# Performance work log

Measured on AMD Instinct MI355X. Metric: run time of the kernel, lower is better.

## Reference

```python
import jax, jax.numpy as jnp
import numpy as np

N_NODES = 1_000_000
N_EDGES = 33_554_432


def setup_inputs() -> dict:
    key = jax.random.key(0)
    k1, k2, k3, k4, k5 = jax.random.split(key, 5)
    node_features = jax.random.normal(k1, (N_NODES,), dtype=jnp.float32)
    edge_index = jax.random.randint(k2, (2, N_EDGES), 0, N_NODES, dtype=jnp.int64)
    cycle_mask = jax.random.uniform(k3, (N_EDGES,), dtype=jnp.float32)
    W = jax.random.normal(k4, (1, 3), dtype=jnp.float32) * 0.5
    b = jax.random.normal(k5, (1,), dtype=jnp.float32) * 0.1
    min_sum_scaler = jnp.array([0.8], dtype=jnp.float32)
    cycle_penalty = jnp.array([-1.0], dtype=jnp.float32)
    return {
        "node_features": node_features,
        "edge_index": edge_index,
        "cycle_mask": cycle_mask,
        "W": W,
        "b": b,
        "min_sum_scaler": min_sum_scaler,
        "cycle_penalty": cycle_penalty,
    }


def reference(node_features, edge_index, cycle_mask, W, b, min_sum_scaler, cycle_penalty):
    src, dst = edge_index[0], edge_index[1]
    x_src = node_features[src]                      # [E] gather
    x_dst = node_features[dst]                      # [E] gather
    # Linear(3,1) over [x_src, x_dst, cycle_mask]: expand the tiny GEMM as fused elementwise
    raw = x_src * W[0, 0] + x_dst * W[0, 1] + cycle_mask * W[0, 2] + b[0]
    raw = jax.nn.leaky_relu(raw, negative_slope=0.01)
    raw = raw + cycle_mask * cycle_penalty[0]
    attention_weights = jax.nn.sigmoid(raw)
    messages = x_src * attention_weights * min_sum_scaler[0]   # [E]
    out = jax.ops.segment_sum(messages, dst, num_segments=node_features.shape[0])
    return out
```

## Files before the change

kernel.cpp:

```cpp
#include <hip/hip_runtime.h>
#include <hip/hip_bf16.h>


#define THREADS 256
#define NBLK    1024
#define NBUCK   256
#define BSH     12
#define NPB     (1 << BSH)
#define TILE    4096
#define NPAD    (NBUCK << BSH)

typedef unsigned int uint4e __attribute__((ext_vector_type(4)));

__device__ __forceinline__ float edge_msg(float xs, float xd, float cc,
                                          float W0, float W1, float W2,
                                          float bb, float ms, float cp) {
    float raw = fmaf(xs, W0, fmaf(xd, W1, fmaf(cc, W2, bb)));
    raw = (raw > 0.0f) ? raw : 0.01f * raw;
    raw = fmaf(cc, cp, raw);
    const float att = __builtin_amdgcn_rcpf(1.0f + __expf(-raw));
    return xs * att * ms;
}

__global__ __launch_bounds__(THREADS) void p1_hist(
    const int* __restrict__ dsts, int E, int epb,
    unsigned int* __restrict__ histT)
{
    __shared__ unsigned int h[4][NBUCK];
    const int t = threadIdx.x;
#pragma unroll
    for (int w = 0; w < 4; ++w) h[w][t] = 0u;
    __syncthreads();

    const int wid   = t >> 6;
    const int blk   = blockIdx.x;
    const int start = blk * epb;
    const int end   = min(E, start + epb);
    const int n     = end - start;
    const int nvec  = n >> 2;

    for (int i = t; i < nvec; i += THREADS) {
        const int4 d4 = *(const int4*)(dsts + start + (i << 2));
        atomicAdd(&h[wid][d4.x >> BSH], 1u);
        atomicAdd(&h[wid][d4.y >> BSH], 1u);
        atomicAdd(&h[wid][d4.z >> BSH], 1u);
        atomicAdd(&h[wid][d4.w >> BSH], 1u);
    }
    for (int e = start + (nvec << 2) + t; e < end; e += THREADS)
        atomicAdd(&h[wid][dsts[e] >> BSH], 1u);

    __syncthreads();
    histT[(size_t)t * NBLK + blk] = h[0][t] + h[1][t] + h[2][t] + h[3][t];
}

__global__ __launch_bounds__(THREADS) void p_scan1(
    unsigned int* __restrict__ histT, unsigned int* __restrict__ totals)
{
    const int b = blockIdx.x;
    unsigned int* row = histT + (size_t)b * NBLK;
    const int t = threadIdx.x;

    uint4 c = *(uint4*)(row + (t << 2));
    const unsigned s1 = c.x;
    const unsigned s2 = c.x + c.y;
    const unsigned s3 = s2 + c.z;
    const unsigned tsum = s3 + c.w;

    __shared__ unsigned int ls[THREADS];
    ls[t] = tsum;
    __syncthreads();
    for (int off = 1; off < THREADS; off <<= 1) {
        unsigned tmp = 0u;
        if (t >= off) tmp = ls[t - off];
        __syncthreads();
        if (t >= off) ls[t] += tmp;
        __syncthreads();
    }
    const unsigned base = (t == 0) ? 0u : ls[t - 1];

    uint4 o;
    o.x = base; o.y = base + s1; o.z = base + s2; o.w = base + s3;
    *(uint4*)(row + (t << 2)) = o;
    if (t == 0) totals[b] = ls[THREADS - 1];
}

__global__ __launch_bounds__(NBUCK) void p_scan2(
    const unsigned int* __restrict__ totals, unsigned int* __restrict__ bucketBase)
{
    __shared__ unsigned int ls[NBUCK];
    const int t = threadIdx.x;
    ls[t] = totals[t];
    __syncthreads();
    for (int off = 1; off < NBUCK; off <<= 1) {
        unsigned tmp = 0u;
        if (t >= off) tmp = ls[t - off];
        __syncthreads();
        if (t >= off) ls[t] += tmp;
        __syncthreads();
    }
    bucketBase[t] = (t == 0) ? 0u : ls[t - 1];
}

__global__ __launch_bounds__(THREADS) void p2_partition(
    const int*   __restrict__ srcs,
    const int*   __restrict__ dsts,
    const float* __restrict__ cm,
    const unsigned int* __restrict__ relT,
    const unsigned int* __restrict__ bucketBase,
    uint2* __restrict__ recs, int E, int epb)
{
    __shared__ unsigned int cur[NBUCK];
    __shared__ unsigned int hist[NBUCK];
    __shared__ unsigned int scanT[NBUCK];
    __shared__ unsigned int rankCur[NBUCK];
    __shared__ unsigned int delta[NBUCK];
    __shared__ uint2        buf[TILE];
    __shared__ unsigned int slotArr[TILE];

    const int blk = blockIdx.x;
    const int t   = threadIdx.x;
    cur[t] = bucketBase[t] + relT[(size_t)t * NBLK + blk];

    const int start = blk * epb;
    const int end   = min(E, start + epb);

    for (int t0 = start; t0 < end; t0 += TILE) {
        const int n    = min(end - t0, TILE);
        const int nvec = n >> 2;

        hist[t] = 0u;
        __syncthreads();
        for (int i = t; i < nvec; i += THREADS) {
            const int4 d4 = *(const int4*)(dsts + t0 + (i << 2));
            atomicAdd(&hist[d4.x >> BSH], 1u);
            atomicAdd(&hist[d4.y >> BSH], 1u);
            atomicAdd(&hist[d4.z >> BSH], 1u);
            atomicAdd(&hist[d4.w >> BSH], 1u);
        }
        for (int e = t0 + (nvec << 2) + t; e < t0 + n; e += THREADS)
            atomicAdd(&hist[dsts[e] >> BSH], 1u);
        __syncthreads();

        scanT[t] = hist[t];
        __syncthreads();
        for (int off = 1; off < NBUCK; off <<= 1) {
            unsigned v = 0u;
            if (t >= off) v = scanT[t - off];
            __syncthreads();
            if (t >= off) scanT[t] += v;
            __syncthreads();
        }
        {
            const unsigned excl = scanT[t] - hist[t];
            rankCur[t] = excl;
            delta[t]   = cur[t] - excl;
        }
        __syncthreads();

        for (int i = t; i < nvec; i += THREADS) {
            const int base = t0 + (i << 2);
            const int4   s4 = *(const int4*)  (srcs + base);
            const int4   d4 = *(const int4*)  (dsts + base);
            const float4 c4 = *(const float4*)(cm   + base);
            const unsigned s[4] = {(unsigned)s4.x, (unsigned)s4.y, (unsigned)s4.z, (unsigned)s4.w};
            const unsigned d[4] = {(unsigned)d4.x, (unsigned)d4.y, (unsigned)d4.z, (unsigned)d4.w};
            const float    c[4] = {c4.x, c4.y, c4.z, c4.w};
#pragma unroll
            for (int k = 0; k < 4; ++k) {
                const unsigned b = d[k] >> BSH;
                const unsigned r = atomicAdd(&rankCur[b], 1u);
                buf[r] = make_uint2((s[k] << BSH) | (d[k] & (NPB - 1u)),
                                    __float_as_uint(c[k]));
                slotArr[r] = r + delta[b];
            }
        }
        for (int e = t0 + (nvec << 2) + t; e < t0 + n; e += THREADS) {
            const unsigned dv = (unsigned)dsts[e];
            const unsigned b  = dv >> BSH;
            const unsigned r  = atomicAdd(&rankCur[b], 1u);
            buf[r] = make_uint2(((unsigned)srcs[e] << BSH) | (dv & (NPB - 1u)),
                                __float_as_uint(cm[e]));
            slotArr[r] = r + delta[b];
        }
        __syncthreads();

        for (int j = t; j < n; j += THREADS)
            recs[slotArr[j]] = buf[j];
        __syncthreads();
        cur[t] += hist[t];
        __syncthreads();
    }
}

__global__ __launch_bounds__(THREADS) void p3_reduce(
    const uint2* __restrict__ recs,
    const unsigned int* __restrict__ totals,
    const unsigned int* __restrict__ bucketBase,
    const float* __restrict__ nf, int N, int nslice,
    const float* __restrict__ Wp, const float* __restrict__ bp,
    const float* __restrict__ msp, const float* __restrict__ cpp_,
    float* __restrict__ partials)
{
    __shared__ float acc[NPB];
    __shared__ float nfw[NPB];
    const int b = blockIdx.x / nslice;
    const int s = blockIdx.x % nslice;
    const int t = threadIdx.x;
    const int nbase = b << BSH;

    for (int j = t; j < NPB; j += THREADS) {
        acc[j] = 0.0f;
        const int g = nbase + j;
        nfw[j] = (g < N) ? nf[g] : 0.0f;
    }
    __syncthreads();

    const float W0 = Wp[0], W1 = Wp[1], W2 = Wp[2];
    const float bb = bp[0], ms = msp[0], cp = cpp_[0];

    const unsigned cnt   = totals[b];
    const unsigned base  = bucketBase[b];
    const unsigned chunk = (cnt + (unsigned)nslice - 1u) / (unsigned)nslice;
    unsigned k0 = min(cnt, (unsigned)s * chunk);
    unsigned k1 = min(cnt, k0 + chunk);
    unsigned g0 = base + k0, g1 = base + k1;

    if ((g0 & 1u) && g0 < g1) {
        if (t == 0) {
            const uint2 r = recs[g0];
            const unsigned dl = r.x & (NPB - 1u);
            atomicAdd(&acc[dl], edge_msg(nf[r.x >> BSH], nfw[dl],
                                         __uint_as_float(r.y),
                                         W0, W1, W2, bb, ms, cp));
        }
        ++g0;
    }
    if (g0 < g1 && ((g1 - g0) & 1u)) {
        --g1;
        if (t == 0) {
            const uint2 r = recs[g1];
            const unsigned dl = r.x & (NPB - 1u);
            atomicAdd(&acc[dl], edge_msg(nf[r.x >> BSH], nfw[dl],
                                         __uint_as_float(r.y),
                                         W0, W1, W2, bb, ms, cp));
        }
    }

    const unsigned npair = (g1 > g0) ? ((g1 - g0) >> 1) : 0u;
    const unsigned noct  = npair >> 2;

    for (unsigned p = t; p < noct; p += THREADS) {
        const uint2* rp = recs + g0 + (p << 3);
        const uint4e qa = __builtin_nontemporal_load((const uint4e*)(rp));
        const uint4e qb = __builtin_nontemporal_load((const uint4e*)(rp + 2));
        const uint4e qc = __builtin_nontemporal_load((const uint4e*)(rp + 4));
        const uint4e qd = __builtin_nontemporal_load((const uint4e*)(rp + 6));
        const float xs0 = nf[qa[0] >> BSH];
        const float xs1 = nf[qa[2] >> BSH];
        const float xs2 = nf[qb[0] >> BSH];
        const float xs3 = nf[qb[2] >> BSH];
        const float xs4 = nf[qc[0] >> BSH];
        const float xs5 = nf[qc[2] >> BSH];
        const float xs6 = nf[qd[0] >> BSH];
        const float xs7 = nf[qd[2] >> BSH];
        const unsigned d0 = qa[0] & (NPB - 1u);
        const unsigned d1 = qa[2] & (NPB - 1u);
        const unsigned d2 = qb[0] & (NPB - 1u);
        const unsigned d3 = qb[2] & (NPB - 1u);
        const unsigned d4 = qc[0] & (NPB - 1u);
        const unsigned d5 = qc[2] & (NPB - 1u);
        const unsigned d6 = qd[0] & (NPB - 1u);
        const unsigned d7 = qd[2] & (NPB - 1u);
        atomicAdd(&acc[d0], edge_msg(xs0, nfw[d0], __uint_as_float(qa[1]), W0, W1, W2, bb, ms, cp));
        atomicAdd(&acc[d1], edge_msg(xs1, nfw[d1], __uint_as_float(qa[3]), W0, W1, W2, bb, ms, cp));
        atomicAdd(&acc[d2], edge_msg(xs2, nfw[d2], __uint_as_float(qb[1]), W0, W1, W2, bb, ms, cp));
        atomicAdd(&acc[d3], edge_msg(xs3, nfw[d3], __uint_as_float(qb[3]), W0, W1, W2, bb, ms, cp));
        atomicAdd(&acc[d4], edge_msg(xs4, nfw[d4], __uint_as_float(qc[1]), W0, W1, W2, bb, ms, cp));
        atomicAdd(&acc[d5], edge_msg(xs5, nfw[d5], __uint_as_float(qc[3]), W0, W1, W2, bb, ms, cp));
        atomicAdd(&acc[d6], edge_msg(xs6, nfw[d6], __uint_as_float(qd[1]), W0, W1, W2, bb, ms, cp));
        atomicAdd(&acc[d7], edge_msg(xs7, nfw[d7], __uint_as_float(qd[3]), W0, W1, W2, bb, ms, cp));
    }

    for (unsigned pp = (noct << 2) + t; pp < npair; pp += THREADS) {
        const uint4e q = __builtin_nontemporal_load((const uint4e*)(recs + g0 + (pp << 1)));
        const float xs0 = nf[q[0] >> BSH];
        const float xs1 = nf[q[2] >> BSH];
        const unsigned dl0 = q[0] & (NPB - 1u);
        const unsigned dl1 = q[2] & (NPB - 1u);
        atomicAdd(&acc[dl0], edge_msg(xs0, nfw[dl0], __uint_as_float(q[1]), W0, W1, W2, bb, ms, cp));
        atomicAdd(&acc[dl1], edge_msg(xs1, nfw[dl1], __uint_as_float(q[3]), W0, W1, W2, bb, ms, cp));
    }
    __syncthreads();

    float* dst = partials + (size_t)s * NPAD + ((size_t)b << BSH);
    for (int j = t << 2; j < NPB; j += THREADS << 2)
        *(float4*)(dst + j) = *(float4*)(acc + j);
}

__global__ __launch_bounds__(THREADS) void p4_sum(
    const float* __restrict__ partials, float* __restrict__ out, int N, int nslice)
{
    const int b4 = (blockIdx.x * blockDim.x + threadIdx.x) << 2;
    if (b4 + 3 < N) {
        float4 a = *(const float4*)(partials + b4);
        for (int s = 1; s < nslice; ++s) {
            const float4 v = *(const float4*)(partials + (size_t)s * NPAD + b4);
            a.x += v.x; a.y += v.y; a.z += v.z; a.w += v.w;
        }
        *(float4*)(out + b4) = a;
    } else if (b4 < N) {
        for (int j = b4; j < N; ++j) {
            float a = 0.0f;
            for (int s = 0; s < nslice; ++s) a += partials[(size_t)s * NPAD + j];
            out[j] = a;
        }
    }
}

__global__ __launch_bounds__(THREADS) void cagat_atomic_fallback(
    const float* __restrict__ nf, const int* __restrict__ srcs,
    const int* __restrict__ dsts, const float* __restrict__ cm,
    const float* __restrict__ Wp, const float* __restrict__ bp,
    const float* __restrict__ msp, const float* __restrict__ cpp_,
    float* __restrict__ out, int E)
{
    const float W0 = Wp[0], W1 = Wp[1], W2 = Wp[2];
    const float bb = bp[0], ms = msp[0], cp = cpp_[0];
    const int i = blockIdx.x * blockDim.x + threadIdx.x;
    for (int e = i; e < E; e += gridDim.x * blockDim.x) {
        const float msg = edge_msg(nf[srcs[e]], nf[dsts[e]], cm[e],
                                   W0, W1, W2, bb, ms, cp);
        atomicAdd(out + dsts[e], msg);
    }
}

extern "C" void kernel_launch(void* const* d_in, const int* in_sizes, int n_in,
                              void* d_out, int out_size, void* d_ws, size_t ws_size,
                              hipStream_t stream) {
    const float* nf   = (const float*)d_in[0];
    const int*   eidx = (const int*)  d_in[1];
    const float* cm   = (const float*)d_in[2];
    const float* W    = (const float*)d_in[3];
    const float* b    = (const float*)d_in[4];
    const float* ms   = (const float*)d_in[5];
    const float* cp   = (const float*)d_in[6];
    float*       out  = (float*)d_out;

    const int E = in_sizes[2];
    const int N = in_sizes[0];
    const int* srcs = eidx;
    const int* dsts = eidx + E;

    const size_t recs_bytes = (size_t)E * 8u;
    const size_t hist_bytes = (size_t)NBUCK * NBLK * 4u;
    const size_t tot_bytes  = 2u * (size_t)NBUCK * 4u;
    const size_t fixed      = recs_bytes + hist_bytes + tot_bytes;

    int nslice = 0;
    if (ws_size >= fixed + (size_t)8 * NPAD * 4u)      nslice = 8;
    else if (ws_size >= fixed + (size_t)4 * NPAD * 4u) nslice = 4;

    if (nslice == 0 || N > NPAD) {
        hipMemsetAsync(d_out, 0, (size_t)out_size * sizeof(float), stream);
        cagat_atomic_fallback<<<8192, THREADS, 0, stream>>>(
            nf, srcs, dsts, cm, W, b, ms, cp, out, E);
        return;
    }

    char* wsb = (char*)d_ws;
    uint2*        recs       = (uint2*)wsb;
    unsigned int* histT      = (unsigned int*)(wsb + recs_bytes);
    unsigned int* totals     = (unsigned int*)(wsb + recs_bytes + hist_bytes);
    unsigned int* bucketBase = totals + NBUCK;
    float*        partials   = (float*)(wsb + fixed);

    const int epb = (E + NBLK - 1) / NBLK;

    p1_hist<<<NBLK, THREADS, 0, stream>>>(dsts, E, epb, histT);
    p_scan1<<<NBUCK, THREADS, 0, stream>>>(histT, totals);
    p_scan2<<<1, NBUCK, 0, stream>>>(totals, bucketBase);
    p2_partition<<<NBLK, THREADS, 0, stream>>>(
        srcs, dsts, cm, histT, bucketBase, recs, E, epb);
    p3_reduce<<<NBUCK * nslice, THREADS, 0, stream>>>(
        recs, totals, bucketBase, nf, N, nslice, W, b, ms, cp, partials);
    p4_sum<<<(N + 4 * THREADS - 1) / (4 * THREADS), THREADS, 0, stream>>>(
        partials, out, N, nslice);
}
```

Before: 853.6 us.

## Merge scan kernels and drop sliced partials so each bucket block writes output

Folds the two scan kernels into one 1024-thread kernel that scans each histogram row with wave shuffles and then scans the bucket totals in shared memory. It also removes the nslice split of p3_reduce and the p4_sum reduction kernel: each of the 256 bucket blocks now processes its whole bucket and writes results straight to the output. This removes two launches and the partials round-trip through memory. In exchange p3_reduce runs only 256 blocks, each handling about 131K edges, which lowers parallelism on a many-CU GPU and may leave CUs idle. The single-block scan also serialises 256 rows over 16 waves.

Result: slower. 884.7 us (+3.6%).

```diff
diff --git a/kernel.cpp b/kernel.cpp
--- a/kernel.cpp
+++ b/kernel.cpp
@@ -53,52 +53,47 @@
     histT[(size_t)t * NBLK + blk] = h[0][t] + h[1][t] + h[2][t] + h[3][t];
 }
 
-__global__ __launch_bounds__(THREADS) void p_scan1(
-    unsigned int* __restrict__ histT, unsigned int* __restrict__ totals)
-{
-    const int b = blockIdx.x;
-    unsigned int* row = histT + (size_t)b * NBLK;
+__global__ __launch_bounds__(1024) void p_scan(
+    unsigned int* __restrict__ histT,
+    unsigned int* __restrict__ totals,
+    unsigned int* __restrict__ bucketBase)
+{
+    __shared__ unsigned int lsT[NBUCK];
     const int t = threadIdx.x;
-
-    uint4 c = *(uint4*)(row + (t << 2));
-    const unsigned s1 = c.x;
-    const unsigned s2 = c.x + c.y;
-    const unsigned s3 = s2 + c.z;
-    const unsigned tsum = s3 + c.w;
-
-    __shared__ unsigned int ls[THREADS];
-    ls[t] = tsum;
-    __syncthreads();
-    for (int off = 1; off < THREADS; off <<= 1) {
-        unsigned tmp = 0u;
-        if (t >= off) tmp = ls[t - off];
-        __syncthreads();
-        if (t >= off) ls[t] += tmp;
-        __syncthreads();
-    }
-    const unsigned base = (t == 0) ? 0u : ls[t - 1];
-
-    uint4 o;
-    o.x = base; o.y = base + s1; o.z = base + s2; o.w = base + s3;
-    *(uint4*)(row + (t << 2)) = o;
-    if (t == 0) totals[b] = ls[THREADS - 1];
-}
-
-__global__ __launch_bounds__(NBUCK) void p_scan2(
-    const unsigned int* __restrict__ totals, unsigned int* __restrict__ bucketBase)
-{
-    __shared__ unsigned int ls[NBUCK];
-    const int t = threadIdx.x;
-    ls[t] = totals[t];
-    __syncthreads();
+    const int w = t >> 6;
+    const int l = t & 63;
+
+    for (int b = w; b < NBUCK; b += 16) {
+        unsigned int* row = histT + (size_t)b * NBLK;
+        unsigned v[16];
+        unsigned s = 0u;
+#pragma unroll
+        for (int k = 0; k < 16; ++k) { v[k] = row[(l << 4) + k]; s += v[k]; }
+        unsigned inc = s;
+#pragma unroll
+        for (int off = 1; off < 64; off <<= 1) {
+            const unsigned u = __shfl_up(inc, off, 64);
+            if (l >= off) inc += u;
+        }
+        unsigned excl = inc - s;
+#pragma unroll
+        for (int k = 0; k < 16; ++k) {
+            const unsigned tmp = v[k];
+            row[(l << 4) + k] = excl;
+            excl += tmp;
+        }
+        if (l == 63) { totals[b] = inc; lsT[b] = inc; }
+    }
+    __syncthreads();
+
     for (int off = 1; off < NBUCK; off <<= 1) {
         unsigned tmp = 0u;
-        if (t >= off) tmp = ls[t - off];
-        __syncthreads();
-        if (t >= off) ls[t] += tmp;
-        __syncthreads();
-    }
-    bucketBase[t] = (t == 0) ? 0u : ls[t - 1];
+        if (t < NBUCK && t >= off) tmp = lsT[t - off];
+        __syncthreads();
+        if (t < NBUCK && t >= off) lsT[t] += tmp;
+        __syncthreads();
+    }
+    if (t < NBUCK) bucketBase[t] = (t == 0) ? 0u : lsT[t - 1];
 }
 
 __global__ __launch_bounds__(THREADS) void p2_partition(
@@ -196,15 +191,14 @@
     const uint2* __restrict__ recs,
     const unsigned int* __restrict__ totals,
     const unsigned int* __restrict__ bucketBase,
-    const float* __restrict__ nf, int N, int nslice,
+    const float* __restrict__ nf, int N,
     const float* __restrict__ Wp, const float* __restrict__ bp,
     const float* __restrict__ msp, const float* __restrict__ cpp_,
-    float* __restrict__ partials)
+    float* __restrict__ out)
 {
     __shared__ float acc[NPB];
     __shared__ float nfw[NPB];
-    const int b = blockIdx.x / nslice;
-    const int s = blockIdx.x % nslice;
+    const int b = blockIdx.x;
     const int t = threadIdx.x;
     const int nbase = b << BSH;
 
@@ -218,12 +212,9 @@
     const float W0 = Wp[0], W1 = Wp[1], W2 = Wp[2];
     const float bb = bp[0], ms = msp[0], cp = cpp_[0];
 
-    const unsigned cnt   = totals[b];
-    const unsigned base  = bucketBase[b];
-    const unsigned chunk = (cnt + (unsigned)nslice - 1u) / (unsigned)nslice;
-    unsigned k0 = min(cnt, (unsigned)s * chunk);
-    unsigned k1 = min(cnt, k0 + chunk);
-    unsigned g0 = base + k0, g1 = base + k1;
+    const unsigned cnt  = totals[b];
+    const unsigned base = bucketBase[b];
+    unsigned g0 = base, g1 = base + cnt;
 
     if ((g0 & 1u) && g0 < g1) {
         if (t == 0) {
@@ -292,27 +283,14 @@
     }
     __syncthreads();
 
-    float* dst = partials + (size_t)s * NPAD + ((size_t)b << BSH);
-    for (int j = t << 2; j < NPB; j += THREADS << 2)
-        *(float4*)(dst + j) = *(float4*)(acc + j);
-}
-
-__global__ __launch_bounds__(THREADS) void p4_sum(
-    const float* __restrict__ partials, float* __restrict__ out, int N, int nslice)
-{
-    const int b4 = (blockIdx.x * blockDim.x + threadIdx.x) << 2;
-    if (b4 + 3 < N) {
-        float4 a = *(const float4*)(partials + b4);
-        for (int s = 1; s < nslice; ++s) {
-            const float4 v = *(const float4*)(partials + (size_t)s * NPAD + b4);
-            a.x += v.x; a.y += v.y; a.z += v.z; a.w += v.w;
-        }
-        *(float4*)(out + b4) = a;
-    } else if (b4 < N) {
-        for (int j = b4; j < N; ++j) {
-            float a = 0.0f;
-            for (int s = 0; s < nslice; ++s) a += partials[(size_t)s * NPAD + j];
-            out[j] = a;
+    for (int j = t << 2; j < NPB; j += THREADS << 2) {
+        const int g = nbase + j;
+        if (g + 3 < N) {
+            *(float4*)(out + g) = *(float4*)(acc + j);
+        } else {
+#pragma unroll
+            for (int k = 0; k < 4; ++k)
+                if (g + k < N) out[g + k] = acc[j + k];
         }
     }
 }
@@ -354,13 +332,9 @@
     const size_t recs_bytes = (size_t)E * 8u;
     const size_t hist_bytes = (size_t)NBUCK * NBLK * 4u;
     const size_t tot_bytes  = 2u * (size_t)NBUCK * 4u;
-    const size_t fixed      = recs_bytes + hist_bytes + tot_bytes;
-
-    int nslice = 0;
-    if (ws_size >= fixed + (size_t)8 * NPAD * 4u)      nslice = 8;
-    else if (ws_size >= fixed + (size_t)4 * NPAD * 4u) nslice = 4;
-
-    if (nslice == 0 || N > NPAD) {
+    const size_t need = recs_bytes + hist_bytes + tot_bytes;
+
+    if (ws_size < need || N > NPAD) {
         hipMemsetAsync(d_out, 0, (size_t)out_size * sizeof(float), stream);
         cagat_atomic_fallback<<<8192, THREADS, 0, stream>>>(
             nf, srcs, dsts, cm, W, b, ms, cp, out, E);
@@ -372,17 +346,13 @@
     unsigned int* histT      = (unsigned int*)(wsb + recs_bytes);
     unsigned int* totals     = (unsigned int*)(wsb + recs_bytes + hist_bytes);
     unsigned int* bucketBase = totals + NBUCK;
-    float*        partials   = (float*)(wsb + fixed);
 
     const int epb = (E + NBLK - 1) / NBLK;
 
     p1_hist<<<NBLK, THREADS, 0, stream>>>(dsts, E, epb, histT);
-    p_scan1<<<NBUCK, THREADS, 0, stream>>>(histT, totals);
-    p_scan2<<<1, NBUCK, 0, stream>>>(totals, bucketBase);
+    p_scan<<<1, 1024, 0, stream>>>(histT, totals, bucketBase);
     p2_partition<<<NBLK, THREADS, 0, stream>>>(
         srcs, dsts, cm, histT, bucketBase, recs, E, epb);
-    p3_reduce<<<NBUCK * nslice, THREADS, 0, stream>>>(
-        recs, totals, bucketBase, nf, N, nslice, W, b, ms, cp, partials);
-    p4_sum<<<(N + 4 * THREADS - 1) / (4 * THREADS), THREADS, 0, stream>>>(
-        partials, out, N, nslice);
-}
+    p3_reduce<<<NBUCK, THREADS, 0, stream>>>(
+        recs, totals, bucketBase, nf, N, W, b, ms, cp, out);
+}
```

## Pack bucket id into cycle-mask bits and drop slice partials in reduce

Applied to the files above, without the earlier changes.

The partition kernel stores the bucket index in the low 8 mantissa bits of the cycle-mask word, removing the shared slot array and recomputing the destination slot during scatter. The reduce stage now uses one block per bucket and writes directly to the output, eliminating per-slice partial buffers and the final summation kernel. This removes a kernel launch and partial traffic but cuts reduce parallelism from 2048 to 256 blocks and slightly truncates cycle_mask precision.

New measurement: 846.9 us. Within noise of the previous version (-0.8%).

```diff
diff --git a/kernel.cpp b/kernel.cpp
--- a/kernel.cpp
+++ b/kernel.cpp
@@ -9,6 +9,7 @@
 #define NPB     (1 << BSH)
 #define TILE    4096
 #define NPAD    (NBUCK << BSH)
+#define CMMASK  0xFFFFFF00u
 
 typedef unsigned int uint4e __attribute__((ext_vector_type(4)));
 
@@ -115,7 +116,6 @@
     __shared__ unsigned int rankCur[NBUCK];
     __shared__ unsigned int delta[NBUCK];
     __shared__ uint2        buf[TILE];
-    __shared__ unsigned int slotArr[TILE];
 
     const int blk = blockIdx.x;
     const int t   = threadIdx.x;
@@ -164,14 +164,14 @@
             const float4 c4 = *(const float4*)(cm   + base);
             const unsigned s[4] = {(unsigned)s4.x, (unsigned)s4.y, (unsigned)s4.z, (unsigned)s4.w};
             const unsigned d[4] = {(unsigned)d4.x, (unsigned)d4.y, (unsigned)d4.z, (unsigned)d4.w};
-            const float    c[4] = {c4.x, c4.y, c4.z, c4.w};
+            const unsigned c[4] = {__float_as_uint(c4.x), __float_as_uint(c4.y),
+                                   __float_as_uint(c4.z), __float_as_uint(c4.w)};
 #pragma unroll
             for (int k = 0; k < 4; ++k) {
                 const unsigned b = d[k] >> BSH;
                 const unsigned r = atomicAdd(&rankCur[b], 1u);
                 buf[r] = make_uint2((s[k] << BSH) | (d[k] & (NPB - 1u)),
-                                    __float_as_uint(c[k]));
-                slotArr[r] = r + delta[b];
+                                    (c[k] & CMMASK) | b);
             }
         }
         for (int e = t0 + (nvec << 2) + t; e < t0 + n; e += THREADS) {
@@ -179,13 +179,14 @@
             const unsigned b  = dv >> BSH;
             const unsigned r  = atomicAdd(&rankCur[b], 1u);
             buf[r] = make_uint2(((unsigned)srcs[e] << BSH) | (dv & (NPB - 1u)),
-                                __float_as_uint(cm[e]));
-            slotArr[r] = r + delta[b];
-        }
-        __syncthreads();
-
-        for (int j = t; j < n; j += THREADS)
-            recs[slotArr[j]] = buf[j];
+                                (__float_as_uint(cm[e]) & CMMASK) | b);
+        }
+        __syncthreads();
+
+        for (int j = t; j < n; j += THREADS) {
+            const uint2 r = buf[j];
+            recs[j + delta[r.y & 0xFFu]] = r;
+        }
         __syncthreads();
         cur[t] += hist[t];
         __syncthreads();
@@ -196,15 +197,14 @@
     const uint2* __restrict__ recs,
     const unsigned int* __restrict__ totals,
     const unsigned int* __restrict__ bucketBase,
-    const float* __restrict__ nf, int N, int nslice,
+    const float* __restrict__ nf, int N,
     const float* __restrict__ Wp, const float* __restrict__ bp,
     const float* __restrict__ msp, const float* __restrict__ cpp_,
-    float* __restrict__ partials)
+    float* __restrict__ out)
 {
     __shared__ float acc[NPB];
     __shared__ float nfw[NPB];
-    const int b = blockIdx.x / nslice;
-    const int s = blockIdx.x % nslice;
+    const int b = blockIdx.x;
     const int t = threadIdx.x;
     const int nbase = b << BSH;
 
@@ -218,19 +218,16 @@
     const float W0 = Wp[0], W1 = Wp[1], W2 = Wp[2];
     const float bb = bp[0], ms = msp[0], cp = cpp_[0];
 
-    const unsigned cnt   = totals[b];
-    const unsigned base  = bucketBase[b];
-    const unsigned chunk = (cnt + (unsigned)nslice - 1u) / (unsigned)nslice;
-    unsigned k0 = min(cnt, (unsigned)s * chunk);
-    unsigned k1 = min(cnt, k0 + chunk);
-    unsigned g0 = base + k0, g1 = base + k1;
+    const unsigned cnt  = totals[b];
+    const unsigned base = bucketBase[b];
+    unsigned g0 = base, g1 = base + cnt;
 
     if ((g0 & 1u) && g0 < g1) {
         if (t == 0) {
             const uint2 r = recs[g0];
             const unsigned dl = r.x & (NPB - 1u);
             atomicAdd(&acc[dl], edge_msg(nf[r.x >> BSH], nfw[dl],
-                                         __uint_as_float(r.y),
+                                         __uint_as_float(r.y & CMMASK),
                                          W0, W1, W2, bb, ms, cp));
         }
         ++g0;
@@ -241,7 +238,7 @@
             const uint2 r = recs[g1];
             const unsigned dl = r.x & (NPB - 1u);
             atomicAdd(&acc[dl], edge_msg(nf[r.x >> BSH], nfw[dl],
-                                         __uint_as_float(r.y),
+                                         __uint_as_float(r.y & CMMASK),
                                          W0, W1, W2, bb, ms, cp));
         }
     }
@@ -271,14 +268,14 @@
         const unsigned d5 = qc[2] & (NPB - 1u);
         const unsigned d6 = qd[0] & (NPB - 1u);
         const unsigned d7 = qd[2] & (NPB - 1u);
-        atomicAdd(&acc[d0], edge_msg(xs0, nfw[d0], __uint_as_float(qa[1]), W0, W1, W2, bb, ms, cp));
-        atomicAdd(&acc[d1], edge_msg(xs1, nfw[d1], __uint_as_float(qa[3]), W0, W1, W2, bb, ms, cp));
-        atomicAdd(&acc[d2], edge_msg(xs2, nfw[d2], __uint_as_float(qb[1]), W0, W1, W2, bb, ms, cp));
-        atomicAdd(&acc[d3], edge_msg(xs3, nfw[d3], __uint_as_float(qb[3]), W0, W1, W2, bb, ms, cp));
-        atomicAdd(&acc[d4], edge_msg(xs4, nfw[d4], __uint_as_float(qc[1]), W0, W1, W2, bb, ms, cp));
-        atomicAdd(&acc[d5], edge_msg(xs5, nfw[d5], __uint_as_float(qc[3]), W0, W1, W2, bb, ms, cp));
-        atomicAdd(&acc[d6], edge_msg(xs6, nfw[d6], __uint_as_float(qd[1]), W0, W1, W2, bb, ms, cp));
-        atomicAdd(&acc[d7], edge_msg(xs7, nfw[d7], __uint_as_float(qd[3]), W0, W1, W2, bb, ms, cp));
+        atomicAdd(&acc[d0], edge_msg(xs0, nfw[d0], __uint_as_float(qa[1] & CMMASK), W0, W1, W2, bb, ms, cp));
+        atomicAdd(&acc[d1], edge_msg(xs1, nfw[d1], __uint_as_float(qa[3] & CMMASK), W0, W1, W2, bb, ms, cp));
+        atomicAdd(&acc[d2], edge_msg(xs2, nfw[d2], __uint_as_float(qb[1] & CMMASK), W0, W1, W2, bb, ms, cp));
+        atomicAdd(&acc[d3], edge_msg(xs3, nfw[d3], __uint_as_float(qb[3] & CMMASK), W0, W1, W2, bb, ms, cp));
+        atomicAdd(&acc[d4], edge_msg(xs4, nfw[d4], __uint_as_float(qc[1] & CMMASK), W0, W1, W2, bb, ms, cp));
+        atomicAdd(&acc[d5], edge_msg(xs5, nfw[d5], __uint_as_float(qc[3] & CMMASK), W0, W1, W2, bb, ms, cp));
+        atomicAdd(&acc[d6], edge_msg(xs6, nfw[d6], __uint_as_float(qd[1] & CMMASK), W0, W1, W2, bb, ms, cp));
+        atomicAdd(&acc[d7], edge_msg(xs7, nfw[d7], __uint_as_float(qd[3] & CMMASK), W0, W1, W2, bb, ms, cp));
     }
 
     for (unsigned pp = (noct << 2) + t; pp < npair; pp += THREADS) {
@@ -287,32 +284,19 @@
         const float xs1 = nf[q[2] >> BSH];
         const unsigned dl0 = q[0] & (NPB - 1u);
         const unsigned dl1 = q[2] & (NPB - 1u);
-        atomicAdd(&acc[dl0], edge_msg(xs0, nfw[dl0], __uint_as_float(q[1]), W0, W1, W2, bb, ms, cp));
-        atomicAdd(&acc[dl1], edge_msg(xs1, nfw[dl1], __uint_as_float(q[3]), W0, W1, W2, bb, ms, cp));
-    }
-    __syncthreads();
-
-    float* dst = partials + (size_t)s * NPAD + ((size_t)b << BSH);
-    for (int j = t << 2; j < NPB; j += THREADS << 2)
-        *(float4*)(dst + j) = *(float4*)(acc + j);
-}
-
-__global__ __launch_bounds__(THREADS) void p4_sum(
-    const float* __restrict__ partials, float* __restrict__ out, int N, int nslice)
-{
-    const int b4 = (blockIdx.x * blockDim.x + threadIdx.x) << 2;
-    if (b4 + 3 < N) {
-        float4 a = *(const float4*)(partials + b4);
-        for (int s = 1; s < nslice; ++s) {
-            const float4 v = *(const float4*)(partials + (size_t)s * NPAD + b4);
-            a.x += v.x; a.y += v.y; a.z += v.z; a.w += v.w;
-        }
-        *(float4*)(out + b4) = a;
-    } else if (b4 < N) {
-        for (int j = b4; j < N; ++j) {
-            float a = 0.0f;
-            for (int s = 0; s < nslice; ++s) a += partials[(size_t)s * NPAD + j];
-            out[j] = a;
+        atomicAdd(&acc[dl0], edge_msg(xs0, nfw[dl0], __uint_as_float(q[1] & CMMASK), W0, W1, W2, bb, ms, cp));
+        atomicAdd(&acc[dl1], edge_msg(xs1, nfw[dl1], __uint_as_float(q[3] & CMMASK), W0, W1, W2, bb, ms, cp));
+    }
+    __syncthreads();
+
+    for (int j = t << 2; j < NPB; j += THREADS << 2) {
+        const int g = nbase + j;
+        if (g + 3 < N) {
+            *(float4*)(out + g) = *(float4*)(acc + j);
+        } else {
+#pragma unroll
+            for (int k = 0; k < 4; ++k)
+                if (g + k < N) out[g + k] = acc[j + k];
         }
     }
 }
@@ -354,13 +338,9 @@
     const size_t recs_bytes = (size_t)E * 8u;
     const size_t hist_bytes = (size_t)NBUCK * NBLK * 4u;
     const size_t tot_bytes  = 2u * (size_t)NBUCK * 4u;
-    const size_t fixed      = recs_bytes + hist_bytes + tot_bytes;
-
-    int nslice = 0;
-    if (ws_size >= fixed + (size_t)8 * NPAD * 4u)      nslice = 8;
-    else if (ws_size >= fixed + (size_t)4 * NPAD * 4u) nslice = 4;
-
-    if (nslice == 0 || N > NPAD) {
+    const size_t need = recs_bytes + hist_bytes + tot_bytes;
+
+    if (ws_size < need || N > NPAD) {
         hipMemsetAsync(d_out, 0, (size_t)out_size * sizeof(float), stream);
         cagat_atomic_fallback<<<8192, THREADS, 0, stream>>>(
             nf, srcs, dsts, cm, W, b, ms, cp, out, E);
@@ -372,7 +352,6 @@
     unsigned int* histT      = (unsigned int*)(wsb + recs_bytes);
     unsigned int* totals     = (unsigned int*)(wsb + recs_bytes + hist_bytes);
     unsigned int* bucketBase = totals + NBUCK;
-    float*        partials   = (float*)(wsb + fixed);
 
     const int epb = (E + NBLK - 1) / NBLK;
 
@@ -381,8 +360,6 @@
     p_scan2<<<1, NBUCK, 0, stream>>>(totals, bucketBase);
     p2_partition<<<NBLK, THREADS, 0, stream>>>(
         srcs, dsts, cm, histT, bucketBase, recs, E, epb);
-    p3_reduce<<<NBUCK * nslice, THREADS, 0, stream>>>(
-        recs, totals, bucketBase, nf, N, nslice, W, b, ms, cp, partials);
-    p4_sum<<<(N + 4 * THREADS - 1) / (4 * THREADS), THREADS, 0, stream>>>(
-        partials, out, N, nslice);
-}
+    p3_reduce<<<NBUCK, THREADS, 0, stream>>>(
+        recs, totals, bucketBase, nf, N, W, b, ms, cp, out);
+}
```
